# Kernel tuning notes

Hardware: AMD Instinct MI355X
Metric: run time of the kernel (lower is better)

## Reference

```python
import jax, jax.numpy as jnp
import numpy as np

V, K, D, RH, RC = 50257, 1024, 1024, 384, 32
B, T = 2, 2048


def setup_inputs() -> dict:
    key = jax.random.key(0)
    k_tok, k_bh, k_bc, k_uh, k_uc = jax.random.split(key, 5)
    return {
        "tokens": jax.random.randint(k_tok, (B, T), 0, V, dtype=jnp.int32),
        "old_to_new": jnp.arange(V, dtype=jnp.int32),  # default hot_ids=arange(K) -> identity perm
        "B_hot": jax.random.normal(k_bh, (RH, D), dtype=jnp.float32) / np.sqrt(RH),
        "B_cold": jax.random.normal(k_bc, (RC, D), dtype=jnp.float32) / np.sqrt(RC),
        "U_hot": jax.random.normal(k_uh, (K, RH), dtype=jnp.float32) / np.sqrt(RH),
        "U_cold": jax.random.normal(k_uc, (V - K, RC), dtype=jnp.float32) / np.sqrt(RC),
        "log_alpha": jnp.zeros((), dtype=jnp.float32),
        "out_bias": jnp.zeros((V,), dtype=jnp.float32),
    }


def reference(tokens, old_to_new, B_hot, B_cold, U_hot, U_cold, log_alpha, out_bias):
    k_hot = U_hot.shape[0]
    # ---- encode: hot/cold masked gather -> low-rank matmul -> select ----
    tok_new = old_to_new[tokens]                       # [B, T]
    is_hot = tok_new < k_hot
    hot_idx = jnp.where(is_hot, tok_new, 0)
    cold_idx = jnp.where(is_hot, 0, tok_new - k_hot)
    emb_hot = U_hot[hot_idx] @ B_hot                   # [B, T, d]
    emb_cold = U_cold[cold_idx] @ B_cold               # [B, T, d]
    latent = jnp.where(is_hot[..., None], emb_hot, emb_cold)
    # ---- decode: tied low-rank logits, block-wise, reorder + scale + bias ----
    alpha = jnp.exp(log_alpha)
    hot_logits = (latent @ B_hot.T) @ U_hot.T          # [B, T, K]
    cold_logits = (latent @ B_cold.T) @ U_cold.T       # [B, T, V-K]
    logits_new = jnp.concatenate([hot_logits, cold_logits], axis=-1)
    logits = jnp.take(logits_new, old_to_new, axis=-1)  # index_select over V
    return logits * alpha + out_bias
```

## Files before the change

kernel.cpp:

```cpp
#include <hip/hip_runtime.h>
#include <hip/hip_bf16.h>

#define VOUT 50257
#define KHOT 1024
#define DIM  1024
#define RHOT 384
#define RCOLD 32
#define RF   416

typedef __attribute__((ext_vector_type(8))) short short8;
typedef __attribute__((ext_vector_type(4))) float f32x4;

__device__ __forceinline__ int delta_row(int n) {
  return (32 - ((17 * n) & 31)) & 31;
}

__global__ void k_convert(const float* __restrict__ Bh, const float* __restrict__ Bc,
                          const float* __restrict__ Uh, const float* __restrict__ Uc,
                          __hip_bfloat16* __restrict__ Bmat,
                          __hip_bfloat16* __restrict__ UhB,
                          __hip_bfloat16* __restrict__ UcB) {
  const int nBh = RHOT * DIM;
  const int nBm = RF * DIM;
  const int nUh = KHOT * RHOT;
  const int nUc = (VOUT - KHOT) * RCOLD;
  const int total = nBm + nUh + nUc;
  for (int i = blockIdx.x * blockDim.x + threadIdx.x; i < total;
       i += gridDim.x * blockDim.x) {
    if (i < nBm) {
      float v = (i < nBh) ? Bh[i] : Bc[i - nBh];
      Bmat[i] = __float2bfloat16(v);
    } else if (i < nBm + nUh) {
      UhB[i - nBm] = __float2bfloat16(Uh[i - nBm]);
    } else {
      int j = i - nBm - nUh;
      UcB[j] = __float2bfloat16(Uc[j]);
    }
  }
}

__global__ __launch_bounds__(256) void k_gram(const __hip_bfloat16* __restrict__ Bmat,
                                              float* __restrict__ G) {
  const int wave = threadIdx.x >> 6;
  const int lane = threadIdx.x & 63;
  const int idx = blockIdx.x * 4 + wave;
  if (idx >= 26 * 26) return;
  const int ti = idx / 26, tj = idx % 26;
  const int i0 = ti * 16, j0 = tj * 16;
  const int col16 = lane & 15;
  const int g4 = lane >> 4;

  f32x4 acc = (f32x4){0.f, 0.f, 0.f, 0.f};
  const __hip_bfloat16* arow = Bmat + (size_t)(i0 + col16) * DIM;
  const __hip_bfloat16* brow = Bmat + (size_t)(j0 + col16) * DIM;
#pragma unroll 4
  for (int ks = 0; ks < DIM / 32; ++ks) {
    short8 a = *reinterpret_cast<const short8*>(arow + ks * 32 + g4 * 8);
    short8 b = *reinterpret_cast<const short8*>(brow + ks * 32 + g4 * 8);
    acc = __builtin_amdgcn_mfma_f32_16x16x32_bf16(a, b, acc, 0, 0, 0);
  }
#pragma unroll
  for (int r = 0; r < 4; ++r)
    G[(size_t)(i0 + g4 * 4 + r) * RF + j0 + col16] = acc[r];
}

__global__ void k_encode(const int* __restrict__ tokens, const int* __restrict__ o2n,
                         const float* __restrict__ Uh, const float* __restrict__ Uc,
                         const float* __restrict__ G, __hip_bfloat16* __restrict__ F) {
  const int n = blockIdx.x;
  __shared__ float u[RHOT];
  const int tok = tokens[n];
  const int tn = o2n[tok];
  const bool hot = tn < KHOT;
  const int R = hot ? RHOT : RCOLD;
  const float* urow = hot ? (Uh + (size_t)tn * RHOT) : (Uc + (size_t)(tn - KHOT) * RCOLD);
  for (int r = threadIdx.x; r < R; r += blockDim.x) u[r] = urow[r];
  __syncthreads();
  const int gbase = hot ? 0 : RHOT;
  for (int c = threadIdx.x; c < RF; c += blockDim.x) {
    float acc = 0.f;
    for (int r = 0; r < R; ++r) acc += u[r] * G[(size_t)(gbase + r) * RF + c];
    F[(size_t)n * RF + c] = __float2bfloat16(acc);
  }
}

#define CPB 256
#define RPB 64
#define NSUB 18
#define EPIT 260

__global__ __launch_bounds__(256) void k_out(const int* __restrict__ o2n,
                                             const __hip_bfloat16* __restrict__ F,
                                             const __hip_bfloat16* __restrict__ Uh,
                                             const __hip_bfloat16* __restrict__ Uc,
                                             const float* __restrict__ log_alpha,
                                             const float* __restrict__ bias,
                                             float* __restrict__ out) {
  __shared__ __hip_bfloat16 Fc[RPB][40];
  __shared__ float Epi[16][EPIT];
  const int tid = threadIdx.x;
  const int wave = tid >> 6;
  const int lane = tid & 63;
  const int col16 = lane & 15;
  const int g4 = lane >> 4;
  const int n0 = blockIdx.y * RPB;
  const int c0 = blockIdx.x * CPB;
  const float alpha = expf(log_alpha[0]);
  const short8 zero8 = (short8){0, 0, 0, 0, 0, 0, 0, 0};

  {
    const int row = tid >> 2, ch = tid & 3;
    *reinterpret_cast<short8*>(&Fc[row][ch * 8]) =
        *reinterpret_cast<const short8*>(F + (size_t)(n0 + row) * RF + RHOT + ch * 8);
  }

  int srcs[5];
  float bv[5];
  short8 bfr[5];
  unsigned hotm = 0, coldm = 0;
#pragma unroll
  for (int i = 0; i < 5; ++i) {
    srcs[i] = KHOT; bv[i] = 0.f; bfr[i] = zero8;
    const int st = wave + 4 * i;
    if (st < NSUB) {
      const int v = c0 + st * 16 + col16;
      const int vc = (v < VOUT) ? v : (VOUT - 1);
      srcs[i] = o2n[vc];
      bv[i] = bias[vc];
      if (__any(srcs[i] < KHOT)) hotm |= (1u << i);
      if (__any(srcs[i] >= KHOT)) coldm |= (1u << i);
      if (srcs[i] >= KHOT)
        bfr[i] = *reinterpret_cast<const short8*>(Uc + (size_t)(srcs[i] - KHOT) * RCOLD + g4 * 8);
    }
  }
  __syncthreads();

  for (int t = 0; t < 4; ++t) {
    int dw[4];
#pragma unroll
    for (int r = 0; r < 4; ++r) dw[r] = delta_row(n0 + t * 16 + g4 * 4 + r);
    const short8 afc = *reinterpret_cast<const short8*>(&Fc[t * 16 + col16][g4 * 8]);

#pragma unroll
    for (int i = 0; i < 5; ++i) {
      const int st = wave + 4 * i;
      if (st >= NSUB) continue;
      f32x4 acc = (f32x4){0.f, 0.f, 0.f, 0.f};
      if (coldm & (1u << i))
        acc = __builtin_amdgcn_mfma_f32_16x16x32_bf16(afc, bfr[i], acc, 0, 0, 0);
      if (hotm & (1u << i)) {
#pragma unroll
        for (int ks = 0; ks < RHOT / 32; ++ks) {
          const short8 afh = *reinterpret_cast<const short8*>(
              F + (size_t)(n0 + t * 16 + col16) * RF + ks * 32 + g4 * 8);
          short8 aw = zero8;
          if (srcs[i] < KHOT)
            aw = *reinterpret_cast<const short8*>(Uh + (size_t)srcs[i] * RHOT + ks * 32 + g4 * 8);
          acc = __builtin_amdgcn_mfma_f32_16x16x32_bf16(afh, aw, acc, 0, 0, 0);
        }
      }
#pragma unroll
      for (int r = 0; r < 4; ++r) {
        const int p = st * 16 + col16 - dw[r];
        if (p >= 0 && p < CPB)
          Epi[g4 * 4 + r][p] = acc[r] * alpha + bv[i];
      }
    }

    asm volatile("s_waitcnt lgkmcnt(0)" ::: "memory");
    __builtin_amdgcn_sched_barrier(0);
    __builtin_amdgcn_s_barrier();
    __builtin_amdgcn_sched_barrier(0);

#pragma unroll
    for (int rr = 0; rr < 4; ++rr) {
      const int row16 = wave * 4 + rr;
      const int n = n0 + t * 16 + row16;
      const int dn = delta_row(n);
      f32x4 vals = *reinterpret_cast<const f32x4*>(&Epi[row16][lane * 4]);
      const int c = c0 + dn + lane * 4;
      const size_t gr = (size_t)n * VOUT;
      if (c + 3 < VOUT) {
        *reinterpret_cast<f32x4*>(out + gr + c) = vals;
      } else {
#pragma unroll
        for (int q = 0; q < 4; ++q)
          if (c + q < VOUT) out[gr + c + q] = vals[q];
      }
    }

    asm volatile("s_waitcnt lgkmcnt(0)" ::: "memory");
    __builtin_amdgcn_sched_barrier(0);
    __builtin_amdgcn_s_barrier();
    __builtin_amdgcn_sched_barrier(0);
  }

  if (blockIdx.x == 0) {
    for (int idx = tid; idx < RPB * 32; idx += 256) {
      const int row = idx >> 5, cc = idx & 31;
      const int n = n0 + row;
      if (cc >= delta_row(n)) continue;
      const int src = o2n[cc];
      float sum = 0.f;
      if (src < KHOT) {
        const __hip_bfloat16* uh = Uh + (size_t)src * RHOT;
        const __hip_bfloat16* fr = F + (size_t)n * RF;
        for (int k = 0; k < RHOT; ++k)
          sum += __bfloat162float(uh[k]) * __bfloat162float(fr[k]);
      } else {
        const __hip_bfloat16* uc = Uc + (size_t)(src - KHOT) * RCOLD;
        const __hip_bfloat16* fr = F + (size_t)n * RF + RHOT;
        for (int k = 0; k < RCOLD; ++k)
          sum += __bfloat162float(uc[k]) * __bfloat162float(fr[k]);
      }
      out[(size_t)n * VOUT + cc] = sum * alpha + bias[cc];
    }
  }
}

extern "C" void kernel_launch(void* const* d_in, const int* in_sizes, int n_in,
                              void* d_out, int out_size, void* d_ws, size_t ws_size,
                              hipStream_t stream) {
  const int* tokens    = (const int*)d_in[0];
  const int* o2n       = (const int*)d_in[1];
  const float* B_hot   = (const float*)d_in[2];
  const float* B_cold  = (const float*)d_in[3];
  const float* U_hot   = (const float*)d_in[4];
  const float* U_cold  = (const float*)d_in[5];
  const float* log_a   = (const float*)d_in[6];
  const float* bias    = (const float*)d_in[7];
  float* out = (float*)d_out;

  const int N = in_sizes[0];

  char* ws = (char*)d_ws;
  __hip_bfloat16* Bmat = (__hip_bfloat16*)(ws + 0);
  __hip_bfloat16* UhB  = (__hip_bfloat16*)(ws + (1u << 20));
  __hip_bfloat16* UcB  = (__hip_bfloat16*)(ws + (2u << 20));
  float*          G    = (float*)(ws + (6u << 20));
  __hip_bfloat16* F    = (__hip_bfloat16*)(ws + (7u << 20));

  k_convert<<<2048, 256, 0, stream>>>(B_hot, B_cold, U_hot, U_cold, Bmat, UhB, UcB);
  k_gram<<<169, 256, 0, stream>>>(Bmat, G);
  k_encode<<<N, 256, 0, stream>>>(tokens, o2n, U_hot, U_cold, G, F);

  dim3 grid((VOUT + CPB - 1) / CPB, N / RPB);
  k_out<<<grid, 256, 0, stream>>>(o2n, F, UhB, UcB, log_a, bias, out);
}
```

Baseline: 373.9 us.

## Make k_out persistent with software-prefetched next chunk staging

```diff
diff --git a/kernel.cpp b/kernel.cpp
--- a/kernel.cpp
+++ b/kernel.cpp
@@ -7,6 +7,8 @@
 #define RHOT 384
 #define RCOLD 32
 #define RF   416
+#define NWIN 197
+#define GRID 1024
 
 typedef __attribute__((ext_vector_type(8))) short short8;
 typedef __attribute__((ext_vector_type(4))) float f32x4;
@@ -84,10 +86,27 @@
   }
 }
 
-#define CPB 256
-#define RPB 64
-#define NSUB 18
-#define EPIT 260
+
+#define STAGE_CHUNK(N0_, C0_, FSL, SRCS, BV, BFR)                                        \
+  do {                                                                                   \
+    {                                                                                    \
+      const int row_ = (tid >> 2) & 15, ch_ = tid & 3;                                   \
+      FSL = *reinterpret_cast<const short8*>(F + (size_t)((N0_) + row_) * RF + RHOT + ch_ * 8); \
+    }                                                                                    \
+    _Pragma("unroll") for (int i_ = 0; i_ < 5; ++i_) {                                   \
+      const int st_ = wave + 4 * i_;                                                     \
+      SRCS[i_] = KHOT; BV[i_] = 0.f; BFR[i_] = zero8;                                    \
+      if (st_ < 18) {                                                                    \
+        const int v_ = (C0_) + st_ * 16 + col16;                                         \
+        const int vc_ = (v_ < VOUT) ? v_ : (VOUT - 1);                                   \
+        SRCS[i_] = o2n[vc_];                                                             \
+        BV[i_] = bias[vc_];                                                              \
+        if (SRCS[i_] >= KHOT)                                                            \
+          BFR[i_] = *reinterpret_cast<const short8*>(                                    \
+              Uc + (size_t)(SRCS[i_] - KHOT) * RCOLD + g4 * 8);                          \
+      }                                                                                  \
+    }                                                                                    \
+  } while (0)
 
 __global__ __launch_bounds__(256) void k_out(const int* __restrict__ o2n,
                                              const __hip_bfloat16* __restrict__ F,
@@ -95,56 +114,55 @@
                                              const __hip_bfloat16* __restrict__ Uc,
                                              const float* __restrict__ log_alpha,
                                              const float* __restrict__ bias,
-                                             float* __restrict__ out) {
-  __shared__ __hip_bfloat16 Fc[RPB][40];
-  __shared__ float Epi[16][EPIT];
+                                             float* __restrict__ out, int totch) {
+  __shared__ __hip_bfloat16 Fc[2][16][40];
+  __shared__ float Epi[16][260];
   const int tid = threadIdx.x;
   const int wave = tid >> 6;
   const int lane = tid & 63;
   const int col16 = lane & 15;
   const int g4 = lane >> 4;
-  const int n0 = blockIdx.y * RPB;
-  const int c0 = blockIdx.x * CPB;
   const float alpha = expf(log_alpha[0]);
   const short8 zero8 = (short8){0, 0, 0, 0, 0, 0, 0, 0};
 
-  {
-    const int row = tid >> 2, ch = tid & 3;
-    *reinterpret_cast<short8*>(&Fc[row][ch * 8]) =
-        *reinterpret_cast<const short8*>(F + (size_t)(n0 + row) * RF + RHOT + ch * 8);
-  }
-
+  int c = blockIdx.x;
+  if (c >= totch) return;
+  int band = c / NWIN, win = c - band * NWIN;
+  int n0 = band * 16, c0 = win * 256;
+
+  short8 fsl;
   int srcs[5];
   float bv[5];
   short8 bfr[5];
-  unsigned hotm = 0, coldm = 0;
-#pragma unroll
-  for (int i = 0; i < 5; ++i) {
-    srcs[i] = KHOT; bv[i] = 0.f; bfr[i] = zero8;
-    const int st = wave + 4 * i;
-    if (st < NSUB) {
-      const int v = c0 + st * 16 + col16;
-      const int vc = (v < VOUT) ? v : (VOUT - 1);
-      srcs[i] = o2n[vc];
-      bv[i] = bias[vc];
-      if (__any(srcs[i] < KHOT)) hotm |= (1u << i);
-      if (__any(srcs[i] >= KHOT)) coldm |= (1u << i);
-      if (srcs[i] >= KHOT)
-        bfr[i] = *reinterpret_cast<const short8*>(Uc + (size_t)(srcs[i] - KHOT) * RCOLD + g4 * 8);
-    }
-  }
-  __syncthreads();
-
-  for (int t = 0; t < 4; ++t) {
-    int dw[4];
-#pragma unroll
-    for (int r = 0; r < 4; ++r) dw[r] = delta_row(n0 + t * 16 + g4 * 4 + r);
-    const short8 afc = *reinterpret_cast<const short8*>(&Fc[t * 16 + col16][g4 * 8]);
-
+  STAGE_CHUNK(n0, c0, fsl, srcs, bv, bfr);
+
+  int buf = 0;
+  for (;;) {
+    if (tid < 64) {
+      const int row = tid >> 2, ch = tid & 3;
+      *reinterpret_cast<short8*>(&Fc[buf][row][ch * 8]) = fsl;
+    }
+    asm volatile("s_waitcnt lgkmcnt(0)" ::: "memory");
+    __builtin_amdgcn_s_barrier();
+
+    unsigned hotm = 0, coldm = 0;
 #pragma unroll
     for (int i = 0; i < 5; ++i) {
       const int st = wave + 4 * i;
-      if (st >= NSUB) continue;
+      if (st < 18) {
+        if (__any(srcs[i] < KHOT)) hotm |= (1u << i);
+        if (__any(srcs[i] >= KHOT)) coldm |= (1u << i);
+      }
+    }
+    int dw[4];
+#pragma unroll
+    for (int r = 0; r < 4; ++r) dw[r] = delta_row(n0 + g4 * 4 + r);
+    const short8 afc = *reinterpret_cast<const short8*>(&Fc[buf][col16][g4 * 8]);
+
+#pragma unroll
+    for (int i = 0; i < 5; ++i) {
+      const int st = wave + 4 * i;
+      if (st >= 18) continue;
       f32x4 acc = (f32x4){0.f, 0.f, 0.f, 0.f};
       if (coldm & (1u << i))
         acc = __builtin_amdgcn_mfma_f32_16x16x32_bf16(afc, bfr[i], acc, 0, 0, 0);
@@ -152,7 +170,7 @@
 #pragma unroll
         for (int ks = 0; ks < RHOT / 32; ++ks) {
           const short8 afh = *reinterpret_cast<const short8*>(
-              F + (size_t)(n0 + t * 16 + col16) * RF + ks * 32 + g4 * 8);
+              F + (size_t)(n0 + col16) * RF + ks * 32 + g4 * 8);
           short8 aw = zero8;
           if (srcs[i] < KHOT)
             aw = *reinterpret_cast<const short8*>(Uh + (size_t)srcs[i] * RHOT + ks * 32 + g4 * 8);
@@ -162,59 +180,75 @@
 #pragma unroll
       for (int r = 0; r < 4; ++r) {
         const int p = st * 16 + col16 - dw[r];
-        if (p >= 0 && p < CPB)
+        if (p >= 0 && p < 256)
           Epi[g4 * 4 + r][p] = acc[r] * alpha + bv[i];
       }
     }
 
+    const int cn = c + GRID;
+    const bool more = cn < totch;
+    int nband = 0, nwin = 0;
+    short8 nfsl = zero8;
+    int nsrcs[5];
+    float nbv[5];
+    short8 nbfr[5];
+#pragma unroll
+    for (int i = 0; i < 5; ++i) { nsrcs[i] = KHOT; nbv[i] = 0.f; nbfr[i] = zero8; }
+    if (more) {
+      nband = cn / NWIN;
+      nwin = cn - nband * NWIN;
+      const int nn0 = nband * 16, nc0 = nwin * 256;
+      STAGE_CHUNK(nn0, nc0, nfsl, nsrcs, nbv, nbfr);
+    }
+
     asm volatile("s_waitcnt lgkmcnt(0)" ::: "memory");
-    __builtin_amdgcn_sched_barrier(0);
     __builtin_amdgcn_s_barrier();
-    __builtin_amdgcn_sched_barrier(0);
 
 #pragma unroll
     for (int rr = 0; rr < 4; ++rr) {
       const int row16 = wave * 4 + rr;
-      const int n = n0 + t * 16 + row16;
+      const int n = n0 + row16;
       const int dn = delta_row(n);
       f32x4 vals = *reinterpret_cast<const f32x4*>(&Epi[row16][lane * 4]);
-      const int c = c0 + dn + lane * 4;
+      const int cc = c0 + dn + lane * 4;
       const size_t gr = (size_t)n * VOUT;
-      if (c + 3 < VOUT) {
-        *reinterpret_cast<f32x4*>(out + gr + c) = vals;
+      if (cc + 3 < VOUT) {
+        *reinterpret_cast<f32x4*>(out + gr + cc) = vals;
       } else {
 #pragma unroll
         for (int q = 0; q < 4; ++q)
-          if (c + q < VOUT) out[gr + c + q] = vals[q];
-      }
-    }
-
-    asm volatile("s_waitcnt lgkmcnt(0)" ::: "memory");
-    __builtin_amdgcn_sched_barrier(0);
-    __builtin_amdgcn_s_barrier();
-    __builtin_amdgcn_sched_barrier(0);
-  }
-
-  if (blockIdx.x == 0) {
-    for (int idx = tid; idx < RPB * 32; idx += 256) {
-      const int row = idx >> 5, cc = idx & 31;
-      const int n = n0 + row;
-      if (cc >= delta_row(n)) continue;
-      const int src = o2n[cc];
-      float sum = 0.f;
-      if (src < KHOT) {
-        const __hip_bfloat16* uh = Uh + (size_t)src * RHOT;
-        const __hip_bfloat16* fr = F + (size_t)n * RF;
-        for (int k = 0; k < RHOT; ++k)
-          sum += __bfloat162float(uh[k]) * __bfloat162float(fr[k]);
-      } else {
-        const __hip_bfloat16* uc = Uc + (size_t)(src - KHOT) * RCOLD;
-        const __hip_bfloat16* fr = F + (size_t)n * RF + RHOT;
-        for (int k = 0; k < RCOLD; ++k)
-          sum += __bfloat162float(uc[k]) * __bfloat162float(fr[k]);
-      }
-      out[(size_t)n * VOUT + cc] = sum * alpha + bias[cc];
-    }
+          if (cc + q < VOUT) out[gr + cc + q] = vals[q];
+      }
+    }
+
+    if (win == 0) {
+      for (int idx = tid; idx < 16 * 32; idx += 256) {
+        const int row = idx >> 5, ccc = idx & 31;
+        const int n = n0 + row;
+        if (ccc >= delta_row(n)) continue;
+        const int src = o2n[ccc];
+        float sum = 0.f;
+        if (src < KHOT) {
+          const __hip_bfloat16* uh = Uh + (size_t)src * RHOT;
+          const __hip_bfloat16* fr = F + (size_t)n * RF;
+          for (int k = 0; k < RHOT; ++k)
+            sum += __bfloat162float(uh[k]) * __bfloat162float(fr[k]);
+        } else {
+          const __hip_bfloat16* uc = Uc + (size_t)(src - KHOT) * RCOLD;
+          const __hip_bfloat16* fr = F + (size_t)n * RF + RHOT;
+          for (int k = 0; k < RCOLD; ++k)
+            sum += __bfloat162float(uc[k]) * __bfloat162float(fr[k]);
+        }
+        out[(size_t)n * VOUT + ccc] = sum * alpha + bias[ccc];
+      }
+    }
+
+    if (!more) break;
+    c = cn; band = nband; win = nwin; n0 = band * 16; c0 = win * 256;
+    fsl = nfsl;
+#pragma unroll
+    for (int i = 0; i < 5; ++i) { srcs[i] = nsrcs[i]; bv[i] = nbv[i]; bfr[i] = nbfr[i]; }
+    buf ^= 1;
   }
 }
 
@@ -244,6 +278,6 @@
   k_gram<<<169, 256, 0, stream>>>(Bmat, G);
   k_encode<<<N, 256, 0, stream>>>(tokens, o2n, U_hot, U_cold, G, F);
 
-  dim3 grid((VOUT + CPB - 1) / CPB, N / RPB);
-  k_out<<<grid, 256, 0, stream>>>(o2n, F, UhB, UcB, log_a, bias, out);
-}
+  const int totch = (N / 16) * NWIN;
+  k_out<<<GRID, 256, 0, stream>>>(o2n, F, UhB, UcB, log_a, bias, out, totch);
+}
```

Result: faster. 364.9 us (-2.4%).
